# Kernel optimization log

Measured on AMD Instinct MI355X. Metric: run time of the kernel, lower is better.

The kernel has to match this reference:

```python
import jax, jax.numpy as jnp
import numpy as np

B, S, D, H = 2, 2048, 1024, 16
DK = D // H


def setup_inputs() -> dict:
    key = jax.random.key(0)
    ks = jax.random.split(key, 11)
    s = 1.0 / np.sqrt(D)
    inp = {
        "q": jax.random.normal(ks[0], (B, S, D), jnp.float32),
        "k": jax.random.normal(ks[1], (B, S, D), jnp.float32),
        "v": jax.random.normal(ks[2], (B, S, D), jnp.float32),
        "mask": jnp.tril(jnp.ones((S, S), jnp.int32))[None, None],  # [1,1,S,S] causal
        "wq": jax.random.normal(ks[3], (D, D), jnp.float32) * s,
        "bq": jax.random.normal(ks[4], (D,), jnp.float32) * s,
        "wk": jax.random.normal(ks[5], (D, D), jnp.float32) * s,
        "bk": jax.random.normal(ks[6], (D,), jnp.float32) * s,
        "wv": jax.random.normal(ks[7], (D, D), jnp.float32) * s,
        "bv": jax.random.normal(ks[8], (D,), jnp.float32) * s,
        "wo": jax.random.normal(ks[9], (D, D), jnp.float32) * s,
        "bo": jax.random.normal(ks[10], (D,), jnp.float32) * s,
    }
    return inp


def reference(q, k, v, mask, wq, bq, wk, bk, wv, bv, wo, bo):
    # Linear projections (torch Linear: x @ W.T + b)
    def split_heads(x):  # [B,S,D] -> [B,H,S,DK]
        return x.reshape(B, S, H, DK).transpose(0, 2, 1, 3)

    query = split_heads(q @ wq.T + bq)
    key_ = split_heads(k @ wk.T + bk)
    value = split_heads(v @ wv.T + bv)

    scale = 1.0 / jnp.sqrt(jnp.asarray(DK, q.dtype))
    scores = jnp.einsum("bhqd,bhkd->bhqk", query, key_) * scale
    scores = jnp.where(mask == 0, jnp.asarray(-1e9, scores.dtype), scores)
    attn = jax.nn.softmax(scores, axis=-1)  # dropout=0.0 -> identity
    x = jnp.einsum("bhqk,bhkd->bhqd", attn, value)
    x = x.transpose(0, 2, 1, 3).reshape(B, S, D)
    return x @ wo.T + bo
```

## Files before the change

### kernel.cpp

```cpp
#include <hip/hip_runtime.h>

typedef unsigned short u16;
typedef __bf16 bf16x8 __attribute__((ext_vector_type(8)));
typedef u16 u16x8 __attribute__((ext_vector_type(8)));
typedef float f32x4 __attribute__((ext_vector_type(4)));

constexpr size_t WQo = 12582912;
constexpr size_t WOo = 15728640;
constexpr size_t QPo = 16777216;
constexpr size_t KPo = 20971520;
constexpr size_t VTo = 25165824;
constexpr size_t OOo = 29360128;

#define GLD(g, l) __builtin_amdgcn_global_load_lds( \
    (const __attribute__((address_space(1))) void*)(g), \
    (__attribute__((address_space(3))) void*)(l), 16, 0, 0)

__device__ __forceinline__ u16 f2bf(float f) {
  unsigned u = __builtin_bit_cast(unsigned, f);
  u += 0x7fffu + ((u >> 16) & 1u);
  return (u16)(u >> 16);
}

__device__ __forceinline__ f32x4 zero4() {
  f32x4 z = {0.f, 0.f, 0.f, 0.f};
  return z;
}

__device__ __forceinline__ f32x4 mfma16(u16x8 a, u16x8 b, f32x4 c) {
  return __builtin_amdgcn_mfma_f32_16x16x32_bf16(
      __builtin_bit_cast(bf16x8, a), __builtin_bit_cast(bf16x8, b), c, 0, 0, 0);
}

__global__ __launch_bounds__(256) void cast_all(
    const float4* __restrict__ q, const float4* __restrict__ k, const float4* __restrict__ v,
    const float4* __restrict__ wq, const float4* __restrict__ wk,
    const float4* __restrict__ wv, const float4* __restrict__ wo,
    ushort4* __restrict__ dst)
{
  int i = blockIdx.x * 256 + threadIdx.x;
  constexpr int QN = 1048576;
  constexpr int WN = 262144;
  float4 val;
  if (i < QN)            val = q[i];
  else if (i < 2 * QN)   val = k[i - QN];
  else if (i < 3 * QN)   val = v[i - 2 * QN];
  else {
    int j = i - 3 * QN;
    if (j < WN)          val = wq[j];
    else if (j < 2 * WN) val = wk[j - WN];
    else if (j < 3 * WN) val = wv[j - 2 * WN];
    else                 val = wo[j - 3 * WN];
  }
  ushort4 o;
  o.x = f2bf(val.x); o.y = f2bf(val.y); o.z = f2bf(val.z); o.w = f2bf(val.w);
  dst[i] = o;
}

template <int TM>
__device__ __forceinline__ void gemm_core(
    const u16* __restrict__ A, const u16* __restrict__ W,
    const float* __restrict__ bias, void* __restrict__ outp,
    int m0, int n0, int mode)
{
  constexpr int Kd = 1024;
  constexpr int BM = TM * 32;
  constexpr int ACALLS = BM / 64;
  __shared__ u16 As[BM * 32];
  __shared__ u16 Bs[128 * 32];
  const int tid = threadIdx.x;
  const int wave = tid >> 6, lane = tid & 63;
  const int q4 = lane >> 4, l15 = lane & 15;
  const int wm = (wave >> 1) * (TM * 16), wn = (wave & 1) * 64;

  f32x4 acc[TM][4];
#pragma unroll
  for (int i = 0; i < TM; ++i)
#pragma unroll
    for (int j = 0; j < 4; ++j) acc[i][j] = zero4();

  for (int kt = 0; kt < Kd; kt += 32) {
#pragma unroll
    for (int t = 0; t < ACALLS; ++t) {
      const int pos = t * 256 + wave * 64 + lane;
      const int lr = pos >> 3, p = pos & 7;
      const int c = p ^ (lr & 7);
      const int m = lr * 2 + (c >> 2), k4 = c & 3;
      GLD(A + (size_t)(m0 + m) * Kd + kt + k4 * 8, As + t * 2048 + wave * 512);
    }
#pragma unroll
    for (int t = 0; t < 2; ++t) {
      const int pos = t * 256 + wave * 64 + lane;
      const int lr = pos >> 3, p = pos & 7;
      const int c = p ^ (lr & 7);
      const int m = lr * 2 + (c >> 2), k4 = c & 3;
      GLD(W + (size_t)(n0 + m) * Kd + kt + k4 * 8, Bs + t * 2048 + wave * 512);
    }
    __syncthreads();
    u16x8 af[TM], bfv[4];
#pragma unroll
    for (int i = 0; i < TM; ++i) {
      const int m = wm + i * 16 + l15;
      const int lr = m >> 1;
      const int p = ((m & 1) * 4 + q4) ^ (lr & 7);
      af[i] = *(const u16x8*)&As[lr * 64 + p * 8];
    }
#pragma unroll
    for (int j = 0; j < 4; ++j) {
      const int m = wn + j * 16 + l15;
      const int lr = m >> 1;
      const int p = ((m & 1) * 4 + q4) ^ (lr & 7);
      bfv[j] = *(const u16x8*)&Bs[lr * 64 + p * 8];
    }
#pragma unroll
    for (int i = 0; i < TM; ++i)
#pragma unroll
      for (int j = 0; j < 4; ++j)
        acc[i][j] = mfma16(af[i], bfv[j], acc[i][j]);
    __syncthreads();
  }

#pragma unroll
  for (int i = 0; i < TM; ++i) {
    const int mb = m0 + wm + i * 16 + q4 * 4;
#pragma unroll
    for (int j = 0; j < 4; ++j) {
      const int col = n0 + wn + j * 16 + l15;
      const float bsv = bias[col];
      if (mode == 1) {
        const int bb = mb >> 11, s = mb & 2047, hh = col >> 6, dk = col & 63;
        ushort4 pk;
        pk.x = f2bf(acc[i][j][0] + bsv);
        pk.y = f2bf(acc[i][j][1] + bsv);
        pk.z = f2bf(acc[i][j][2] + bsv);
        pk.w = f2bf(acc[i][j][3] + bsv);
        *(ushort4*)&((u16*)outp)[((size_t)(bb * 16 + hh) * 64 + dk) * 2048 + s] = pk;
      } else {
#pragma unroll
        for (int r = 0; r < 4; ++r) {
          const float val = acc[i][j][r] + bsv;
          const int m = mb + r;
          if (mode == 0) {
            const int bb = m >> 11, s = m & 2047, hh = col >> 6, dk = col & 63;
            ((u16*)outp)[((size_t)(bb * 16 + hh) * 2048 + s) * 64 + dk] = f2bf(val);
          } else {
            ((float*)outp)[(size_t)m * 1024 + col] = val;
          }
        }
      }
    }
  }
}

__global__ __launch_bounds__(256) void proj_gemm(
    u16* __restrict__ ws, const float* __restrict__ bq,
    const float* __restrict__ bk, const float* __restrict__ bv)
{
  const int id = blockIdx.x;
  const int z = id >> 8, rem = id & 255;
  const int bx = rem >> 5, by = rem & 31;
  const u16* A = ws + (size_t)z * 4194304;
  const u16* W = ws + WQo + (size_t)z * 1048576;
  const float* bias = (z == 0) ? bq : ((z == 1) ? bk : bv);
  u16* outp = ws + QPo + (size_t)z * 4194304;
  gemm_core<4>(A, W, bias, outp, by * 128, bx * 128, (z == 2) ? 1 : 0);
}

__global__ __launch_bounds__(256) void out_gemm(
    const u16* __restrict__ ws, const float* __restrict__ bo, float* __restrict__ out)
{
  const int id = blockIdx.x;
  const int bx = id >> 6, by = id & 63;
  gemm_core<2>(ws + OOo, ws + WOo, bo, out, by * 64, bx * 128, 3);
}

__global__ __launch_bounds__(256) void flash_attn(u16* __restrict__ ws)
{
  constexpr int S = 2048;
  const int a = blockIdx.x;
  const int b = 31 - blockIdx.x;
  const int bh = blockIdx.y;
  const int bb = bh >> 4, h = bh & 15;
  const int tid = threadIdx.x;
  const int wave = tid >> 6, lane = tid & 63;
  const int q4 = lane >> 4, l15 = lane & 15;

  __shared__ u16 QsA[64 * 64];
  __shared__ u16 QsB[64 * 64];
  __shared__ u16 Ks[2][64 * 64];
  __shared__ u16 Vs[2][64 * 64];

  const u16* Qg = ws + QPo + (size_t)bh * S * 64;
  const u16* Kg = ws + KPo + (size_t)bh * S * 64;
  const u16* Vg = ws + VTo + (size_t)bh * 64 * S;
  u16* Og = ws + OOo;

  const int ch0 = wave * 128 + lane;
  const int ch1 = ch0 + 64;
  const int r0 = ch0 >> 3, c0 = (ch0 & 7) ^ (r0 & 7);
  const int r1 = ch1 >> 3, c1 = (ch1 & 7) ^ (r1 & 7);

  GLD(Qg + (size_t)(a * 64 + r0) * 64 + c0 * 8, QsA + wave * 1024);
  GLD(Qg + (size_t)(a * 64 + r1) * 64 + c1 * 8, QsA + wave * 1024 + 512);
  GLD(Qg + (size_t)(b * 64 + r0) * 64 + c0 * 8, QsB + wave * 1024);
  GLD(Qg + (size_t)(b * 64 + r1) * 64 + c1 * 8, QsB + wave * 1024 + 512);
  GLD(Kg + (size_t)r0 * 64 + c0 * 8, Ks[0] + wave * 1024);
  GLD(Kg + (size_t)r1 * 64 + c1 * 8, Ks[0] + wave * 1024 + 512);
  GLD(Vg + (size_t)r0 * S + c0 * 8, Vs[0] + wave * 1024);
  GLD(Vg + (size_t)r1 * S + c1 * 8, Vs[0] + wave * 1024 + 512);
  __syncthreads();

  u16x8 qfA[2], qfB[2];
  {
    const int row = wave * 16 + l15;
#pragma unroll
    for (int kk = 0; kk < 2; ++kk) {
      const int c = (kk * 4 + q4) ^ (row & 7);
      qfA[kk] = *(const u16x8*)&QsA[row * 64 + c * 8];
      qfB[kk] = *(const u16x8*)&QsB[row * 64 + c * 8];
    }
  }
  u16* Ps = QsA + wave * 1024;

  f32x4 oA[4], oB[4];
  float lA[4], lB[4];
#pragma unroll
  for (int j = 0; j < 4; ++j) { oA[j] = zero4(); oB[j] = zero4(); }
#pragma unroll
  for (int r = 0; r < 4; ++r) { lA[r] = 0.f; lB[r] = 0.f; }

  for (int kt = 0; kt <= b; ++kt) {
    const u16* Ksb = Ks[kt & 1];
    const u16* Vsb = Vs[kt & 1];
    if (kt < b) {
      const u16* Kt = Kg + (size_t)(kt + 1) * 64 * 64;
      u16* Kd = Ks[(kt + 1) & 1];
      u16* Vd = Vs[(kt + 1) & 1];
      GLD(Kt + (size_t)r0 * 64 + c0 * 8, Kd + wave * 1024);
      GLD(Kt + (size_t)r1 * 64 + c1 * 8, Kd + wave * 1024 + 512);
      GLD(Vg + (size_t)r0 * S + (kt + 1) * 64 + c0 * 8, Vd + wave * 1024);
      GLD(Vg + (size_t)r1 * S + (kt + 1) * 64 + c1 * 8, Vd + wave * 1024 + 512);
    }

    auto process = [&](const u16x8* qf, f32x4* o_acc, float* l_p, int qt, bool diag) {
      f32x4 sf[4];
#pragma unroll
      for (int j = 0; j < 4; ++j) {
        f32x4 z = zero4();
        const int row = j * 16 + l15;
#pragma unroll
        for (int kk = 0; kk < 2; ++kk) {
          const int c = (kk * 4 + q4) ^ (row & 7);
          z = mfma16(qf[kk], *(const u16x8*)&Ksb[row * 64 + c * 8], z);
        }
        sf[j] = z;
      }
      if (diag) {
        const int rowg0 = qt * 64 + wave * 16 + q4 * 4;
#pragma unroll
        for (int j = 0; j < 4; ++j) {
          const int colg = kt * 64 + j * 16 + l15;
#pragma unroll
          for (int r = 0; r < 4; ++r) {
            float val = sf[j][r] * 0.125f;
            if (colg > rowg0 + r) val = -__builtin_inff();
            sf[j][r] = __expf(val);
          }
        }
      } else {
#pragma unroll
        for (int j = 0; j < 4; ++j)
#pragma unroll
          for (int r = 0; r < 4; ++r)
            sf[j][r] = __expf(sf[j][r] * 0.125f);
      }
#pragma unroll
      for (int j = 0; j < 4; ++j)
#pragma unroll
        for (int r = 0; r < 4; ++r) l_p[r] += sf[j][r];

#pragma unroll
      for (int j = 0; j < 4; ++j)
#pragma unroll
        for (int r = 0; r < 4; ++r) {
          const int m = q4 * 4 + r;
          const int srow = j * 16 + l15;
          const int pos = m * 64 + (((srow >> 3) ^ (m & 7)) << 3) + (srow & 7);
          Ps[pos] = f2bf(sf[j][r]);
        }
      u16x8 pf[2];
#pragma unroll
      for (int kk = 0; kk < 2; ++kk) {
        const int c = (kk * 4 + q4) ^ (l15 & 7);
        pf[kk] = *(const u16x8*)&Ps[l15 * 64 + c * 8];
      }
#pragma unroll
      for (int j = 0; j < 4; ++j) {
        const int row = j * 16 + l15;
#pragma unroll
        for (int kk = 0; kk < 2; ++kk) {
          const int c = (kk * 4 + q4) ^ (row & 7);
          o_acc[j] = mfma16(pf[kk], *(const u16x8*)&Vsb[row * 64 + c * 8], o_acc[j]);
        }
      }
    };

    process(qfB, oB, lB, b, kt == b);
    if (kt <= a) process(qfA, oA, lA, a, kt == a);
    __syncthreads();
  }

#pragma unroll
  for (int off = 1; off < 16; off <<= 1)
#pragma unroll
    for (int r = 0; r < 4; ++r) {
      lA[r] += __shfl_xor(lA[r], off, 64);
      lB[r] += __shfl_xor(lB[r], off, 64);
    }

#pragma unroll
  for (int r = 0; r < 4; ++r) {
    const float invA = 1.f / lA[r];
    const float invB = 1.f / lB[r];
    const int sA = a * 64 + wave * 16 + q4 * 4 + r;
    const int sB = b * 64 + wave * 16 + q4 * 4 + r;
    const size_t baseA = ((size_t)(bb * 2048 + sA)) * 1024 + h * 64;
    const size_t baseB = ((size_t)(bb * 2048 + sB)) * 1024 + h * 64;
#pragma unroll
    for (int j = 0; j < 4; ++j) {
      Og[baseA + j * 16 + l15] = f2bf(oA[j][r] * invA);
      Og[baseB + j * 16 + l15] = f2bf(oB[j][r] * invB);
    }
  }
}

extern "C" void kernel_launch(void* const* d_in, const int* in_sizes, int n_in,
                              void* d_out, int out_size, void* d_ws, size_t ws_size,
                              hipStream_t stream)
{
  const float* q  = (const float*)d_in[0];
  const float* k  = (const float*)d_in[1];
  const float* v  = (const float*)d_in[2];
  const float* wq = (const float*)d_in[4];
  const float* bq = (const float*)d_in[5];
  const float* wk = (const float*)d_in[6];
  const float* bk = (const float*)d_in[7];
  const float* wv = (const float*)d_in[8];
  const float* bv = (const float*)d_in[9];
  const float* wo = (const float*)d_in[10];
  const float* bo = (const float*)d_in[11];
  u16* ws = (u16*)d_ws;
  float* out = (float*)d_out;

  cast_all<<<16384, 256, 0, stream>>>(
      (const float4*)q, (const float4*)k, (const float4*)v,
      (const float4*)wq, (const float4*)wk, (const float4*)wv, (const float4*)wo,
      (ushort4*)ws);
  proj_gemm<<<768, 256, 0, stream>>>(ws, bq, bk, bv);
  flash_attn<<<dim3(16, 32), 256, 0, stream>>>(ws);
  out_gemm<<<512, 256, 0, stream>>>(ws, bo, out);
}
```

Before: 237.8 us.

## Fuse fp32-to-bf16 activation cast into projection GEMM A-tile loads

The separate cast pass over q/k/v activations is removed. The projection GEMM now loads fp32 activation tiles directly into LDS (with swizzle) and converts them to bf16 when reading fragments, while only the weights are still pre-cast. This avoids writing and rereading bf16 copies of the inputs. In exchange it doubles the LDS footprint and global traffic for the A tiles, and the conversion is redone for each N-tile block.

```diff
diff --git a/kernel.cpp b/kernel.cpp
--- a/kernel.cpp
+++ b/kernel.cpp
@@ -32,42 +32,40 @@
       __builtin_bit_cast(bf16x8, a), __builtin_bit_cast(bf16x8, b), c, 0, 0, 0);
 }
 
-__global__ __launch_bounds__(256) void cast_all(
-    const float4* __restrict__ q, const float4* __restrict__ k, const float4* __restrict__ v,
+__device__ __forceinline__ u16x8 cvt8(f32x4 lo, f32x4 hi) {
+  u16x8 r;
+  r[0] = f2bf(lo[0]); r[1] = f2bf(lo[1]); r[2] = f2bf(lo[2]); r[3] = f2bf(lo[3]);
+  r[4] = f2bf(hi[0]); r[5] = f2bf(hi[1]); r[6] = f2bf(hi[2]); r[7] = f2bf(hi[3]);
+  return r;
+}
+
+__global__ __launch_bounds__(256) void cast_w(
     const float4* __restrict__ wq, const float4* __restrict__ wk,
     const float4* __restrict__ wv, const float4* __restrict__ wo,
     ushort4* __restrict__ dst)
 {
   int i = blockIdx.x * 256 + threadIdx.x;
-  constexpr int QN = 1048576;
   constexpr int WN = 262144;
   float4 val;
-  if (i < QN)            val = q[i];
-  else if (i < 2 * QN)   val = k[i - QN];
-  else if (i < 3 * QN)   val = v[i - 2 * QN];
-  else {
-    int j = i - 3 * QN;
-    if (j < WN)          val = wq[j];
-    else if (j < 2 * WN) val = wk[j - WN];
-    else if (j < 3 * WN) val = wv[j - 2 * WN];
-    else                 val = wo[j - 3 * WN];
-  }
+  if (i < WN)          val = wq[i];
+  else if (i < 2 * WN) val = wk[i - WN];
+  else if (i < 3 * WN) val = wv[i - 2 * WN];
+  else                 val = wo[i - 3 * WN];
   ushort4 o;
   o.x = f2bf(val.x); o.y = f2bf(val.y); o.z = f2bf(val.z); o.w = f2bf(val.w);
   dst[i] = o;
 }
 
-template <int TM>
+template <int TM, bool AF32>
 __device__ __forceinline__ void gemm_core(
-    const u16* __restrict__ A, const u16* __restrict__ W,
+    const void* __restrict__ Ap, const u16* __restrict__ W,
     const float* __restrict__ bias, void* __restrict__ outp,
     int m0, int n0, int mode)
 {
   constexpr int Kd = 1024;
   constexpr int BM = TM * 32;
-  constexpr int ACALLS = BM / 64;
-  __shared__ u16 As[BM * 32];
-  __shared__ u16 Bs[128 * 32];
+  __shared__ alignas(16) u16 As[AF32 ? BM * 64 : BM * 32];
+  __shared__ alignas(16) u16 Bs[128 * 32];
   const int tid = threadIdx.x;
   const int wave = tid >> 6, lane = tid & 63;
   const int q4 = lane >> 4, l15 = lane & 15;
@@ -80,13 +78,27 @@
     for (int j = 0; j < 4; ++j) acc[i][j] = zero4();
 
   for (int kt = 0; kt < Kd; kt += 32) {
-#pragma unroll
-    for (int t = 0; t < ACALLS; ++t) {
-      const int pos = t * 256 + wave * 64 + lane;
-      const int lr = pos >> 3, p = pos & 7;
-      const int c = p ^ (lr & 7);
-      const int m = lr * 2 + (c >> 2), k4 = c & 3;
-      GLD(A + (size_t)(m0 + m) * Kd + kt + k4 * 8, As + t * 2048 + wave * 512);
+    if (AF32) {
+      const float* Af = (const float*)Ap;
+#pragma unroll
+      for (int t = 0; t < BM / 32; ++t) {
+        const int pos = t * 256 + wave * 64 + lane;
+        const int row = pos >> 3, p = pos & 7;
+        const int c = p ^ (row & 7);
+        GLD(Af + (size_t)(m0 + row) * Kd + kt + c * 4,
+            As + (size_t)(t * 256 + wave * 64) * 8);
+      }
+    } else {
+      const u16* Ab = (const u16*)Ap;
+#pragma unroll
+      for (int t = 0; t < BM / 64; ++t) {
+        const int pos = t * 256 + wave * 64 + lane;
+        const int lr = pos >> 3, p = pos & 7;
+        const int c = p ^ (lr & 7);
+        const int m = lr * 2 + (c >> 2), k4 = c & 3;
+        GLD(Ab + (size_t)(m0 + m) * Kd + kt + k4 * 8,
+            As + (size_t)(t * 256 + wave * 64) * 8);
+      }
     }
 #pragma unroll
     for (int t = 0; t < 2; ++t) {
@@ -94,16 +106,26 @@
       const int lr = pos >> 3, p = pos & 7;
       const int c = p ^ (lr & 7);
       const int m = lr * 2 + (c >> 2), k4 = c & 3;
-      GLD(W + (size_t)(n0 + m) * Kd + kt + k4 * 8, Bs + t * 2048 + wave * 512);
+      GLD(W + (size_t)(n0 + m) * Kd + kt + k4 * 8,
+          Bs + (size_t)(t * 256 + wave * 64) * 8);
     }
     __syncthreads();
     u16x8 af[TM], bfv[4];
 #pragma unroll
     for (int i = 0; i < TM; ++i) {
       const int m = wm + i * 16 + l15;
-      const int lr = m >> 1;
-      const int p = ((m & 1) * 4 + q4) ^ (lr & 7);
-      af[i] = *(const u16x8*)&As[lr * 64 + p * 8];
+      if (AF32) {
+        const float* Asf = (const float*)As;
+        const int p0 = (2 * q4) ^ (m & 7);
+        const int p1 = p0 ^ 1;
+        f32x4 lo = *(const f32x4*)&Asf[m * 32 + p0 * 4];
+        f32x4 hi = *(const f32x4*)&Asf[m * 32 + p1 * 4];
+        af[i] = cvt8(lo, hi);
+      } else {
+        const int lr = m >> 1;
+        const int p = ((m & 1) * 4 + q4) ^ (lr & 7);
+        af[i] = *(const u16x8*)&As[lr * 64 + p * 8];
+      }
     }
 #pragma unroll
     for (int j = 0; j < 4; ++j) {
@@ -153,17 +175,19 @@
 }
 
 __global__ __launch_bounds__(256) void proj_gemm(
-    u16* __restrict__ ws, const float* __restrict__ bq,
-    const float* __restrict__ bk, const float* __restrict__ bv)
+    const float* __restrict__ q, const float* __restrict__ k,
+    const float* __restrict__ v, u16* __restrict__ ws,
+    const float* __restrict__ bq, const float* __restrict__ bk,
+    const float* __restrict__ bv)
 {
   const int id = blockIdx.x;
   const int z = id >> 8, rem = id & 255;
   const int bx = rem >> 5, by = rem & 31;
-  const u16* A = ws + (size_t)z * 4194304;
+  const float* A = (z == 0) ? q : ((z == 1) ? k : v);
   const u16* W = ws + WQo + (size_t)z * 1048576;
   const float* bias = (z == 0) ? bq : ((z == 1) ? bk : bv);
   u16* outp = ws + QPo + (size_t)z * 4194304;
-  gemm_core<4>(A, W, bias, outp, by * 128, bx * 128, (z == 2) ? 1 : 0);
+  gemm_core<4, true>(A, W, bias, outp, by * 128, bx * 128, (z == 2) ? 1 : 0);
 }
 
 __global__ __launch_bounds__(256) void out_gemm(
@@ -171,7 +195,7 @@
 {
   const int id = blockIdx.x;
   const int bx = id >> 6, by = id & 63;
-  gemm_core<2>(ws + OOo, ws + WOo, bo, out, by * 64, bx * 128, 3);
+  gemm_core<2, false>(ws + OOo, ws + WOo, bo, out, by * 64, bx * 128, 3);
 }
 
 __global__ __launch_bounds__(256) void flash_attn(u16* __restrict__ ws)
@@ -352,11 +376,10 @@
   u16* ws = (u16*)d_ws;
   float* out = (float*)d_out;
 
-  cast_all<<<16384, 256, 0, stream>>>(
-      (const float4*)q, (const float4*)k, (const float4*)v,
+  cast_w<<<4096, 256, 0, stream>>>(
       (const float4*)wq, (const float4*)wk, (const float4*)wv, (const float4*)wo,
-      (ushort4*)ws);
-  proj_gemm<<<768, 256, 0, stream>>>(ws, bq, bk, bv);
+      (ushort4*)(ws + WQo));
+  proj_gemm<<<768, 256, 0, stream>>>(q, k, v, ws, bq, bk, bv);
   flash_attn<<<dim3(16, 32), 256, 0, stream>>>(ws);
   out_gemm<<<512, 256, 0, stream>>>(ws, bo, out);
 }
```

Measured after the change: 267.6 us. 1.13x slower.

## Double-buffer LDS tiles in projection GEMM to overlap loads with MFMA

Applied to the files above, without the earlier changes.

The projection GEMM core now uses two LDS buffers for the A and W tiles. It issues the global-to-LDS loads for the next k-step before computing on the current one, which removes one barrier per iteration. Address and swizzle offsets are precomputed once outside the loop to cut per-iteration integer math. In exchange it doubles LDS usage, which may lower occupancy. The loop relies on a single barrier to separate buffer reuse from the async loads.

```diff
diff --git a/kernel.cpp b/kernel.cpp
--- a/kernel.cpp
+++ b/kernel.cpp
@@ -65,59 +65,83 @@
 {
   constexpr int Kd = 1024;
   constexpr int BM = TM * 32;
-  constexpr int ACALLS = BM / 64;
-  __shared__ u16 As[BM * 32];
-  __shared__ u16 Bs[128 * 32];
+  constexpr int AC = BM / 64;
+  constexpr int ASZ = BM * 32;
+  __shared__ alignas(16) u16 As[2 * ASZ];
+  __shared__ alignas(16) u16 Bs[2 * 4096];
   const int tid = threadIdx.x;
   const int wave = tid >> 6, lane = tid & 63;
   const int q4 = lane >> 4, l15 = lane & 15;
   const int wm = (wave >> 1) * (TM * 16), wn = (wave & 1) * 64;
 
+  const u16* asrc[AC]; int adst[AC];
+#pragma unroll
+  for (int t = 0; t < AC; ++t) {
+    const int pos = t * 256 + tid;
+    const int lr = pos >> 3, p = pos & 7;
+    const int c = p ^ (lr & 7);
+    asrc[t] = A + (size_t)(m0 + lr * 2 + (c >> 2)) * Kd + (c & 3) * 8;
+    adst[t] = pos * 8;
+  }
+  const u16* bsrc[2]; int bdst[2];
+#pragma unroll
+  for (int t = 0; t < 2; ++t) {
+    const int pos = t * 256 + tid;
+    const int lr = pos >> 3, p = pos & 7;
+    const int c = p ^ (lr & 7);
+    bsrc[t] = W + (size_t)(n0 + lr * 2 + (c >> 2)) * Kd + (c & 3) * 8;
+    bdst[t] = pos * 8;
+  }
+  int aoff[TM], boff[4];
+#pragma unroll
+  for (int i = 0; i < TM; ++i) {
+    const int m = wm + i * 16 + l15;
+    const int lr = m >> 1;
+    const int p = ((m & 1) * 4 + q4) ^ (lr & 7);
+    aoff[i] = lr * 64 + p * 8;
+  }
+#pragma unroll
+  for (int j = 0; j < 4; ++j) {
+    const int m = wn + j * 16 + l15;
+    const int lr = m >> 1;
+    const int p = ((m & 1) * 4 + q4) ^ (lr & 7);
+    boff[j] = lr * 64 + p * 8;
+  }
+
   f32x4 acc[TM][4];
 #pragma unroll
   for (int i = 0; i < TM; ++i)
 #pragma unroll
     for (int j = 0; j < 4; ++j) acc[i][j] = zero4();
 
-  for (int kt = 0; kt < Kd; kt += 32) {
-#pragma unroll
-    for (int t = 0; t < ACALLS; ++t) {
-      const int pos = t * 256 + wave * 64 + lane;
-      const int lr = pos >> 3, p = pos & 7;
-      const int c = p ^ (lr & 7);
-      const int m = lr * 2 + (c >> 2), k4 = c & 3;
-      GLD(A + (size_t)(m0 + m) * Kd + kt + k4 * 8, As + t * 2048 + wave * 512);
-    }
-#pragma unroll
-    for (int t = 0; t < 2; ++t) {
-      const int pos = t * 256 + wave * 64 + lane;
-      const int lr = pos >> 3, p = pos & 7;
-      const int c = p ^ (lr & 7);
-      const int m = lr * 2 + (c >> 2), k4 = c & 3;
-      GLD(W + (size_t)(n0 + m) * Kd + kt + k4 * 8, Bs + t * 2048 + wave * 512);
-    }
+#pragma unroll
+  for (int t = 0; t < AC; ++t) GLD(asrc[t], As + adst[t]);
+#pragma unroll
+  for (int t = 0; t < 2; ++t) GLD(bsrc[t], Bs + bdst[t]);
+
+  for (int it = 0; it < 32; ++it) {
+    const int buf = it & 1;
     __syncthreads();
+    if (it < 31) {
+      const int kt = (it + 1) * 32;
+      const int ob = buf ^ 1;
+#pragma unroll
+      for (int t = 0; t < AC; ++t) GLD(asrc[t] + kt, As + ob * ASZ + adst[t]);
+#pragma unroll
+      for (int t = 0; t < 2; ++t) GLD(bsrc[t] + kt, Bs + ob * 4096 + bdst[t]);
+    }
+    const u16* Ab = As + buf * ASZ;
+    const u16* Bb = Bs + buf * 4096;
     u16x8 af[TM], bfv[4];
 #pragma unroll
-    for (int i = 0; i < TM; ++i) {
-      const int m = wm + i * 16 + l15;
-      const int lr = m >> 1;
-      const int p = ((m & 1) * 4 + q4) ^ (lr & 7);
-      af[i] = *(const u16x8*)&As[lr * 64 + p * 8];
-    }
-#pragma unroll
-    for (int j = 0; j < 4; ++j) {
-      const int m = wn + j * 16 + l15;
-      const int lr = m >> 1;
-      const int p = ((m & 1) * 4 + q4) ^ (lr & 7);
-      bfv[j] = *(const u16x8*)&Bs[lr * 64 + p * 8];
-    }
+    for (int i = 0; i < TM; ++i) af[i] = *(const u16x8*)&Ab[aoff[i]];
+#pragma unroll
+    for (int j = 0; j < 4; ++j) bfv[j] = *(const u16x8*)&Bb[boff[j]];
 #pragma unroll
     for (int i = 0; i < TM; ++i)
 #pragma unroll
       for (int j = 0; j < 4; ++j)
         acc[i][j] = mfma16(af[i], bfv[j], acc[i][j]);
-    __syncthreads();
   }
 
 #pragma unroll
```

New measurement: 230.3 us. 3.2% less time.
